# Performance work log

Hardware: AMD Instinct MI355X
Metric: run time of the kernel (lower is better)

Reference implementation:

```python
import jax, jax.numpy as jnp
import numpy as np

NUM_HEADS = 8


def conv2x2_s2(x, w, b):
    # x: [B,C,H,W], w: [O,I,2,2], stride 2, no padding (torch Conv2d k=2,s=2)
    y = jax.lax.conv_general_dilated(
        x, w, window_strides=(2, 2), padding='VALID',
        dimension_numbers=('NCHW', 'OIHW', 'NCHW'))
    return y + b[None, :, None, None]


def up2(x):
    return jnp.repeat(jnp.repeat(x, 2, axis=2), 2, axis=3)


def setup_inputs() -> dict:
    key = jax.random.key(0)
    B, C, H, W = 1, 128, 64, 64
    N = H * W
    ks = jax.random.split(key, 7)
    p = lambda k, shape: jax.random.normal(k, shape, jnp.float32) * 0.02
    return {
        'x': jax.random.normal(ks[0], (B, N, C), jnp.float32),
        'conv1_w': p(ks[1], (C, C, 2, 2)),
        'conv1_b': jnp.zeros((C,), jnp.float32),
        'conv2_w': p(ks[2], (C, C, 2, 2)),
        'conv2_b': jnp.zeros((C,), jnp.float32),
        'q_w': p(ks[3], (C, C)),
        'kv_w': p(ks[4], (2 * C, C)),
        'proj_w': p(ks[5], (C, C)),
        'proj_b': jnp.zeros((C,), jnp.float32),
        'H': H,
        'W': W,
    }


def reference(x, conv1_w, conv1_b, conv2_w, conv2_b, q_w, kv_w, proj_w, proj_b, H, W):
    B, N, C = x.shape
    hd = C // NUM_HEADS
    scale = hd ** -0.5
    # tokens -> feature map
    x_ = x.transpose(0, 2, 1).reshape(B, C, H, W)
    # ChannelPriorQueries: conv(s2) -> up2 -> conv(s2) -> up2 (HxW preserved)
    tq = up2(conv2x2_s2(up2(conv2x2_s2(x_, conv1_w, conv1_b)), conv2_w, conv2_b))
    tq = tq.reshape(B, C, N).transpose(0, 2, 1)  # [B,N,C]
    # projections (torch Linear: y = x @ W.T)
    q = (tq @ q_w.T).reshape(B, N, NUM_HEADS, hd).transpose(0, 2, 1, 3)   # [B,h,N,d]
    kv = (x @ kv_w.T).reshape(B, N, 2, NUM_HEADS, hd).transpose(2, 0, 3, 1, 4)
    k, v = kv[0], kv[1]  # [B,h,N,d]
    # sr_ratio == 1: F.interpolate(q, size=(N, d)) is the identity
    attn = jax.nn.softmax(jnp.einsum('bhqd,bhkd->bhqk', q, k) * scale, axis=-1)
    out = jnp.einsum('bhqk,bhkd->bhqd', attn, v)
    out = out.transpose(0, 2, 1, 3).reshape(B, N, C)
    return out @ proj_w.T + proj_b
```

## Files before the change

### kernel.cpp

```cpp
#include <hip/hip_runtime.h>
#include <hip/hip_bf16.h>

#define CCH 128
#define NTOK 4096
#define NP 1024
#define NH 8
#define HD 16

typedef __attribute__((ext_vector_type(8)))  short s8v;
typedef __attribute__((ext_vector_type(16))) float f32x16;

#define OFF_Y1T   0
#define OFF_M     131072
#define OFF_QB    147456
#define OFF_AT16  147584
#define OFF_K16   180352
#define OFF_VT16  442496

__device__ inline unsigned short f2bf(float v) {
    __hip_bfloat16 b = __float2bfloat16(v);
    return *reinterpret_cast<unsigned short*>(&b);
}
__device__ inline unsigned int pk2bf(float a, float b) {
    __hip_bfloat162 t = __float22bfloat162_rn(make_float2(a, b));
    return *reinterpret_cast<unsigned int*>(&t);
}
__device__ inline int crow_of(int r, int hi) { return (r & 3) + 8*(r >> 2) + 4*hi; }

union BU { unsigned int u[4]; s8v v; };

__global__ void __launch_bounds__(256) kA_prep(const float* __restrict__ x,
        const float* __restrict__ w1, const float* __restrict__ b1,
        const float* __restrict__ w2, const float* __restrict__ b2,
        const float* __restrict__ qw, const float* __restrict__ kvw,
        float* __restrict__ ws,
        unsigned short* __restrict__ k16, unsigned short* __restrict__ vt16) {
    __shared__ float smem[2048];
    const int b = blockIdx.x;
    const int tid = threadIdx.x;
    const int w = tid >> 6, lane = tid & 63;
    const int ql = lane & 31, hi = lane >> 5;

    if (b < 256) {
        const int n0 = (b >> 1) * 32;
        const int octile = (b & 1) * 4 + w;
        const int oc0 = octile * 32;
        const bool isK = (octile < 4);
        const float* arow = (isK ? x + (n0 + ql)*CCH : kvw + (oc0 + ql)*CCH) + hi*8;
        const float* brow = (isK ? kvw + (oc0 + ql)*CCH : x + (n0 + ql)*CCH) + hi*8;
        f32x16 acc = {};
        float4 a0 = *reinterpret_cast<const float4*>(arow);
        float4 a1 = *reinterpret_cast<const float4*>(arow + 4);
        float4 b0 = *reinterpret_cast<const float4*>(brow);
        float4 b1 = *reinterpret_cast<const float4*>(brow + 4);
        for (int kk = 0; kk < 8; ++kk) {
            float4 na0 = a0, na1 = a1, nb0 = b0, nb1 = b1;
            if (kk < 7) {
                na0 = *reinterpret_cast<const float4*>(arow + (kk+1)*16);
                na1 = *reinterpret_cast<const float4*>(arow + (kk+1)*16 + 4);
                nb0 = *reinterpret_cast<const float4*>(brow + (kk+1)*16);
                nb1 = *reinterpret_cast<const float4*>(brow + (kk+1)*16 + 4);
            }
            BU au, bu;
            au.u[0] = pk2bf(a0.x, a0.y); au.u[1] = pk2bf(a0.z, a0.w);
            au.u[2] = pk2bf(a1.x, a1.y); au.u[3] = pk2bf(a1.z, a1.w);
            bu.u[0] = pk2bf(b0.x, b0.y); bu.u[1] = pk2bf(b0.z, b0.w);
            bu.u[2] = pk2bf(b1.x, b1.y); bu.u[3] = pk2bf(b1.z, b1.w);
            acc = __builtin_amdgcn_mfma_f32_32x32x16_bf16(au.v, bu.v, acc, 0, 0, 0);
            a0 = na0; a1 = na1; b0 = nb0; b1 = nb1;
        }
        if (isK) {
            const int oc = oc0 + ql, h = oc >> 4, d = oc & 15;
            #pragma unroll
            for (int r = 0; r < 16; ++r) {
                const int n = n0 + crow_of(r, hi);
                k16[(h*NTOK + n)*HD + d] = f2bf(acc[r]);
            }
        } else {
            #pragma unroll
            for (int r = 0; r < 16; ++r) {
                const int oc = oc0 + crow_of(r, hi);
                vt16[(oc - CCH)*NTOK + n0 + ql] = f2bf(acc[r]);
            }
        }
    } else if (b < 512) {
        const int pp = tid >> 7, o = tid & 127;
        float* xs = smem + pp * 1024;
        const int p0 = (b - 256) * 4 + pp * 2;
        #pragma unroll
        for (int pl = 0; pl < 2; ++pl) {
            int p = p0 + pl;
            int i = p >> 5, j = p & 31;
            int t00 = (2*i)*64 + 2*j;
            float4 v;
            v.x = x[(t00     )*CCH + o];
            v.y = x[(t00 +  1)*CCH + o];
            v.z = x[(t00 + 64)*CCH + o];
            v.w = x[(t00 + 65)*CCH + o];
            *reinterpret_cast<float4*>(&xs[(pl*CCH + o)*4]) = v;
        }
        __syncthreads();
        float acc0 = 0.f, acc1 = 0.f;
        for (int c = 0; c < CCH; ++c) {
            float4 w4 = *reinterpret_cast<const float4*>(&w1[(o*CCH + c)*4]);
            float4 a  = *reinterpret_cast<const float4*>(&xs[c*4]);
            float4 bq = *reinterpret_cast<const float4*>(&xs[(CCH + c)*4]);
            acc0 += w4.x*a.x + w4.y*a.y + w4.z*a.z + w4.w*a.w;
            acc1 += w4.x*bq.x + w4.y*bq.y + w4.z*bq.z + w4.w*bq.w;
        }
        ws[OFF_Y1T + (p0+0)*CCH + o] = acc0 + b1[o];
        ws[OFF_Y1T + (p0+1)*CCH + o] = acc1 + b1[o];
    } else {
        int id = (b - 512) * 256 + tid;
        int r = id >> 7, c = id & 127;
        float acc = 0.f;
        for (int o = 0; o < CCH; ++o) {
            float4 w4 = *reinterpret_cast<const float4*>(&w2[(o*CCH + c)*4]);
            acc += qw[r*CCH + o] * (w4.x + w4.y + w4.z + w4.w);
        }
        ws[OFF_M + id] = acc * 0.25f;
        if (id < CCH) {
            float a = 0.f;
            for (int o = 0; o < CCH; ++o) a += qw[id*CCH + o] * b2[o];
            ws[OFF_QB + id] = a * 0.25f;
        }
    }
}

__global__ void __launch_bounds__(1024) kB_attn(const float* __restrict__ ws,
                                                const unsigned short* __restrict__ k16,
                                                const unsigned short* __restrict__ vt16,
                                                unsigned short* __restrict__ at16) {
    __shared__ float ys[32*CCH];
    __shared__ unsigned short qs[32*24];
    __shared__ float oacc[16*HD*32];
    __shared__ float lbuf[16*32];
    const int tid = threadIdx.x;
    const int h = blockIdx.x >> 5, qt = blockIdx.x & 31;

    reinterpret_cast<float4*>(ys)[tid] =
        reinterpret_cast<const float4*>(ws + OFF_Y1T + qt*32*CCH)[tid];
    __syncthreads();

    {
        const int qq = tid >> 5, r = (tid >> 1) & 15, half = tid & 1;
        const float* Mr = ws + OFF_M + (h*HD + r)*CCH + half*64;
        const float* yr = ys + qq*CCH + half*64;
        float a = 0.f;
        #pragma unroll
        for (int c4 = 0; c4 < 16; ++c4) {
            float4 m4 = *reinterpret_cast<const float4*>(Mr + c4*4);
            float4 y4 = *reinterpret_cast<const float4*>(yr + c4*4);
            a += m4.x*y4.x + m4.y*y4.y + m4.z*y4.z + m4.w*y4.w;
        }
        a += __shfl_xor(a, 1);
        if (half == 0) qs[qq*24 + r] = f2bf(a + ws[OFF_QB + h*HD + r]);
    }
    __syncthreads();

    const int s = tid >> 6;
    const int lane = tid & 63;
    const int ql = lane & 31;
    const int hi = lane >> 5;

    s8v qf = *reinterpret_cast<const s8v*>(qs + ql*24 + hi*8);

    const unsigned short* kp = k16 + (h*NTOK)*HD;
    const unsigned short* vp = vt16 + (h*HD + ql)*NTOK;
    const bool vvalid = (ql < HD);

    f32x16 acc = {};
    float lsum = 0.f;

    const int kbase = s*256;
    s8v kf = *reinterpret_cast<const s8v*>(kp + (kbase + ql)*HD + hi*8);
    s8v vf1 = {}, vf2 = {};
    if (vvalid) {
        vf1 = *reinterpret_cast<const s8v*>(vp + kbase + hi*8);
        vf2 = *reinterpret_cast<const s8v*>(vp + kbase + 16 + hi*8);
    }

    for (int c = 0; c < 8; ++c) {
        s8v kf_n = kf, vf1_n = vf1, vf2_n = vf2;
        if (c < 7) {
            const int kb2 = kbase + (c+1)*32;
            kf_n = *reinterpret_cast<const s8v*>(kp + (kb2 + ql)*HD + hi*8);
            if (vvalid) {
                vf1_n = *reinterpret_cast<const s8v*>(vp + kb2 + hi*8);
                vf2_n = *reinterpret_cast<const s8v*>(vp + kb2 + 16 + hi*8);
            }
        }

        f32x16 z = {};
        f32x16 st = __builtin_amdgcn_mfma_f32_32x32x16_bf16(kf, qf, z, 0, 0, 0);

        float p[16];
        float ls = 0.f;
        #pragma unroll
        for (int r = 0; r < 16; ++r) { p[r] = __expf(st[r]); ls += p[r]; }
        lsum += ls;

        unsigned int W[8];
        #pragma unroll
        for (int i = 0; i < 8; ++i) W[i] = pk2bf(p[2*i], p[2*i+1]);

        BU b1x, b2x;
        {
            unsigned int s0 = (unsigned int)__shfl_xor((int)W[0], 32);
            unsigned int s1 = (unsigned int)__shfl_xor((int)W[1], 32);
            unsigned int s2 = (unsigned int)__shfl_xor((int)W[2], 32);
            unsigned int s3 = (unsigned int)__shfl_xor((int)W[3], 32);
            b1x.u[0] = hi ? s2 : W[0];
            b1x.u[1] = hi ? s3 : W[1];
            b1x.u[2] = hi ? W[2] : s0;
            b1x.u[3] = hi ? W[3] : s1;
            unsigned int s4 = (unsigned int)__shfl_xor((int)W[4], 32);
            unsigned int s5 = (unsigned int)__shfl_xor((int)W[5], 32);
            unsigned int s6 = (unsigned int)__shfl_xor((int)W[6], 32);
            unsigned int s7 = (unsigned int)__shfl_xor((int)W[7], 32);
            b2x.u[0] = hi ? s6 : W[4];
            b2x.u[1] = hi ? s7 : W[5];
            b2x.u[2] = hi ? W[6] : s4;
            b2x.u[3] = hi ? W[7] : s5;
        }

        acc = __builtin_amdgcn_mfma_f32_32x32x16_bf16(vf1, b1x.v, acc, 0, 0, 0);
        acc = __builtin_amdgcn_mfma_f32_32x32x16_bf16(vf2, b2x.v, acc, 0, 0, 0);

        kf = kf_n; vf1 = vf1_n; vf2 = vf2_n;
    }

    float lt = lsum + __shfl_xor(lsum, 32);
    if (lane < 32) lbuf[s*32 + ql] = lt;
    #pragma unroll
    for (int r = 0; r < 8; ++r) {
        int d = crow_of(r, hi);
        oacc[(s*HD + d)*32 + ql] = acc[r];
    }
    __syncthreads();

    if (tid < 512) {
        const int q2 = tid & 31, d2 = tid >> 5;
        float ltot = 0.f, o = 0.f;
        #pragma unroll
        for (int ss = 0; ss < 16; ++ss) {
            ltot += lbuf[ss*32 + q2];
            o    += oacc[(ss*HD + d2)*32 + q2];
        }
        at16[(qt*32 + q2)*CCH + h*HD + d2] = f2bf(o / ltot);
    }
}

__global__ void __launch_bounds__(256) k5_proj(const unsigned short* __restrict__ at16,
                                               const float* __restrict__ pw,
                                               const float* __restrict__ pb,
                                               float* __restrict__ out) {
    const int ptile = blockIdx.x;
    const int w = threadIdx.x >> 6, lane = threadIdx.x & 63;
    const int ql = lane & 31, hi = lane >> 5;
    const int oc0 = w * 32;
    const unsigned short* arow = at16 + (ptile*32 + ql)*CCH + hi*8;
    const float* brow = pw + (oc0 + ql)*CCH + hi*8;

    f32x16 acc = {};
    s8v af = *reinterpret_cast<const s8v*>(arow);
    float4 b0 = *reinterpret_cast<const float4*>(brow);
    float4 b1 = *reinterpret_cast<const float4*>(brow + 4);
    for (int kk = 0; kk < 8; ++kk) {
        s8v naf = af; float4 nb0 = b0, nb1 = b1;
        if (kk < 7) {
            naf = *reinterpret_cast<const s8v*>(arow + (kk+1)*16);
            nb0 = *reinterpret_cast<const float4*>(brow + (kk+1)*16);
            nb1 = *reinterpret_cast<const float4*>(brow + (kk+1)*16 + 4);
        }
        BU bu;
        bu.u[0] = pk2bf(b0.x, b0.y); bu.u[1] = pk2bf(b0.z, b0.w);
        bu.u[2] = pk2bf(b1.x, b1.y); bu.u[3] = pk2bf(b1.z, b1.w);
        acc = __builtin_amdgcn_mfma_f32_32x32x16_bf16(af, bu.v, acc, 0, 0, 0);
        af = naf; b0 = nb0; b1 = nb1;
    }

    const float bias = pb[oc0 + ql];
    #pragma unroll
    for (int r = 0; r < 16; ++r) {
        const int j = crow_of(r, hi);
        const int t00 = 128*ptile + 2*j;
        const float v = acc[r] + bias;
        out[(t00     )*CCH + oc0 + ql] = v;
        out[(t00 +  1)*CCH + oc0 + ql] = v;
        out[(t00 + 64)*CCH + oc0 + ql] = v;
        out[(t00 + 65)*CCH + oc0 + ql] = v;
    }
}

extern "C" void kernel_launch(void* const* d_in, const int* in_sizes, int n_in,
                              void* d_out, int out_size, void* d_ws, size_t ws_size,
                              hipStream_t stream) {
    const float* x   = (const float*)d_in[0];
    const float* w1  = (const float*)d_in[1];
    const float* b1  = (const float*)d_in[2];
    const float* w2  = (const float*)d_in[3];
    const float* b2  = (const float*)d_in[4];
    const float* qw  = (const float*)d_in[5];
    const float* kvw = (const float*)d_in[6];
    const float* pw  = (const float*)d_in[7];
    const float* pb  = (const float*)d_in[8];
    float* ws  = (float*)d_ws;
    float* out = (float*)d_out;

    unsigned short* at16 = (unsigned short*)(ws + OFF_AT16);
    unsigned short* k16  = (unsigned short*)(ws + OFF_K16);
    unsigned short* vt16 = (unsigned short*)(ws + OFF_VT16);

    hipLaunchKernelGGL(kA_prep, dim3(576), dim3(256), 0, stream,
                       x, w1, b1, w2, b2, qw, kvw, ws, k16, vt16);
    hipLaunchKernelGGL(kB_attn, dim3(256), dim3(1024), 0, stream,
                       ws, k16, vt16, at16);
    hipLaunchKernelGGL(k5_proj, dim3(32), dim3(256), 0, stream, at16, pw, pb, out);
}
```

Baseline: 53.10 us.

## Split attention keys across two blocks and merge partial sums in projection

The attention kernel now launches 512 blocks of 512 threads instead of 256 blocks of 1024. Each block handles half of the key range and writes unnormalized partial outputs and row sums in fp32 to workspace. The projection kernel adds the two halves, normalizes, converts to bf16 and runs the GEMM. The aim is more blocks to fill the CUs and a smaller per-block reduction, at the cost of extra fp32 partial traffic, duplicated query-projection work per block, and a projection kernel that no longer prefetches its inputs.

```diff
diff --git a/kernel.cpp b/kernel.cpp
--- a/kernel.cpp
+++ b/kernel.cpp
@@ -13,9 +13,10 @@
 #define OFF_Y1T   0
 #define OFF_M     131072
 #define OFF_QB    147456
-#define OFF_AT16  147584
-#define OFF_K16   180352
-#define OFF_VT16  442496
+#define OFF_ATP   147584
+#define OFF_LP    409728
+#define OFF_K16   426112
+#define OFF_VT16  688256
 
 __device__ inline unsigned short f2bf(float v) {
     __hip_bfloat16 b = __float2bfloat16(v);
@@ -52,9 +53,9 @@
         float4 a0 = *reinterpret_cast<const float4*>(arow);
         float4 a1 = *reinterpret_cast<const float4*>(arow + 4);
         float4 b0 = *reinterpret_cast<const float4*>(brow);
-        float4 b1 = *reinterpret_cast<const float4*>(brow + 4);
+        float4 b1v = *reinterpret_cast<const float4*>(brow + 4);
         for (int kk = 0; kk < 8; ++kk) {
-            float4 na0 = a0, na1 = a1, nb0 = b0, nb1 = b1;
+            float4 na0 = a0, na1 = a1, nb0 = b0, nb1 = b1v;
             if (kk < 7) {
                 na0 = *reinterpret_cast<const float4*>(arow + (kk+1)*16);
                 na1 = *reinterpret_cast<const float4*>(arow + (kk+1)*16 + 4);
@@ -65,9 +66,9 @@
             au.u[0] = pk2bf(a0.x, a0.y); au.u[1] = pk2bf(a0.z, a0.w);
             au.u[2] = pk2bf(a1.x, a1.y); au.u[3] = pk2bf(a1.z, a1.w);
             bu.u[0] = pk2bf(b0.x, b0.y); bu.u[1] = pk2bf(b0.z, b0.w);
-            bu.u[2] = pk2bf(b1.x, b1.y); bu.u[3] = pk2bf(b1.z, b1.w);
+            bu.u[2] = pk2bf(b1v.x, b1v.y); bu.u[3] = pk2bf(b1v.z, b1v.w);
             acc = __builtin_amdgcn_mfma_f32_32x32x16_bf16(au.v, bu.v, acc, 0, 0, 0);
-            a0 = na0; a1 = na1; b0 = nb0; b1 = nb1;
+            a0 = na0; a1 = na1; b0 = nb0; b1v = nb1;
         }
         if (isK) {
             const int oc = oc0 + ql, h = oc >> 4, d = oc & 15;
@@ -127,34 +128,37 @@
     }
 }
 
-__global__ void __launch_bounds__(1024) kB_attn(const float* __restrict__ ws,
-                                                const unsigned short* __restrict__ k16,
-                                                const unsigned short* __restrict__ vt16,
-                                                unsigned short* __restrict__ at16) {
-    __shared__ float ys[32*CCH];
-    __shared__ unsigned short qs[32*24];
-    __shared__ float oacc[16*HD*32];
-    __shared__ float lbuf[16*32];
+__global__ void __launch_bounds__(512) kB_attn(const float* __restrict__ ws,
+                                               const unsigned short* __restrict__ k16,
+                                               const unsigned short* __restrict__ vt16,
+                                               float* __restrict__ atp,
+                                               float* __restrict__ lp) {
+    __shared__ float smem[8832];
+    float* ys = smem;
+    unsigned short* qs = (unsigned short*)(smem + 4096);
+    float* oacc = smem + 4480;
+    float* lbuf = smem + 8576;
     const int tid = threadIdx.x;
-    const int h = blockIdx.x >> 5, qt = blockIdx.x & 31;
-
-    reinterpret_cast<float4*>(ys)[tid] =
-        reinterpret_cast<const float4*>(ws + OFF_Y1T + qt*32*CCH)[tid];
+    const int h = blockIdx.x >> 6, qt = (blockIdx.x >> 1) & 31, kh = blockIdx.x & 1;
+
+    #pragma unroll
+    for (int e = 0; e < 8; ++e)
+        reinterpret_cast<float4*>(ys)[tid + 512*e] =
+            reinterpret_cast<const float4*>(ws + OFF_Y1T + qt*32*CCH)[tid + 512*e];
     __syncthreads();
 
     {
-        const int qq = tid >> 5, r = (tid >> 1) & 15, half = tid & 1;
-        const float* Mr = ws + OFF_M + (h*HD + r)*CCH + half*64;
-        const float* yr = ys + qq*CCH + half*64;
+        const int qq = tid >> 4, r = tid & 15;
+        const float* Mr = ws + OFF_M + (h*HD + r)*CCH;
+        const float* yr = ys + qq*CCH;
         float a = 0.f;
         #pragma unroll
-        for (int c4 = 0; c4 < 16; ++c4) {
+        for (int c4 = 0; c4 < 32; ++c4) {
             float4 m4 = *reinterpret_cast<const float4*>(Mr + c4*4);
             float4 y4 = *reinterpret_cast<const float4*>(yr + c4*4);
             a += m4.x*y4.x + m4.y*y4.y + m4.z*y4.z + m4.w*y4.w;
         }
-        a += __shfl_xor(a, 1);
-        if (half == 0) qs[qq*24 + r] = f2bf(a + ws[OFF_QB + h*HD + r]);
+        qs[qq*24 + r] = f2bf(a + ws[OFF_QB + h*HD + r]);
     }
     __syncthreads();
 
@@ -172,7 +176,7 @@
     f32x16 acc = {};
     float lsum = 0.f;
 
-    const int kbase = s*256;
+    const int kbase = kh*2048 + s*256;
     s8v kf = *reinterpret_cast<const s8v*>(kp + (kbase + ql)*HD + hi*8);
     s8v vf1 = {}, vf2 = {};
     if (vvalid) {
@@ -239,19 +243,22 @@
     }
     __syncthreads();
 
-    if (tid < 512) {
+    {
         const int q2 = tid & 31, d2 = tid >> 5;
         float ltot = 0.f, o = 0.f;
         #pragma unroll
-        for (int ss = 0; ss < 16; ++ss) {
+        for (int ss = 0; ss < 8; ++ss) {
             ltot += lbuf[ss*32 + q2];
             o    += oacc[(ss*HD + d2)*32 + q2];
         }
-        at16[(qt*32 + q2)*CCH + h*HD + d2] = f2bf(o / ltot);
-    }
-}
-
-__global__ void __launch_bounds__(256) k5_proj(const unsigned short* __restrict__ at16,
+        const int p = qt*32 + q2;
+        atp[kh*(NP*CCH) + p*CCH + h*HD + d2] = o;
+        if (d2 == 0) lp[kh*(NP*NH) + p*NH + h] = ltot;
+    }
+}
+
+__global__ void __launch_bounds__(256) k5_proj(const float* __restrict__ atp,
+                                               const float* __restrict__ lp,
                                                const float* __restrict__ pw,
                                                const float* __restrict__ pb,
                                                float* __restrict__ out) {
@@ -259,25 +266,30 @@
     const int w = threadIdx.x >> 6, lane = threadIdx.x & 63;
     const int ql = lane & 31, hi = lane >> 5;
     const int oc0 = w * 32;
-    const unsigned short* arow = at16 + (ptile*32 + ql)*CCH + hi*8;
+    const int p = ptile*32 + ql;
     const float* brow = pw + (oc0 + ql)*CCH + hi*8;
 
     f32x16 acc = {};
-    s8v af = *reinterpret_cast<const s8v*>(arow);
-    float4 b0 = *reinterpret_cast<const float4*>(brow);
-    float4 b1 = *reinterpret_cast<const float4*>(brow + 4);
     for (int kk = 0; kk < 8; ++kk) {
-        s8v naf = af; float4 nb0 = b0, nb1 = b1;
-        if (kk < 7) {
-            naf = *reinterpret_cast<const s8v*>(arow + (kk+1)*16);
-            nb0 = *reinterpret_cast<const float4*>(brow + (kk+1)*16);
-            nb1 = *reinterpret_cast<const float4*>(brow + (kk+1)*16 + 4);
-        }
+        const float l = lp[p*NH + kk] + lp[NP*NH + p*NH + kk];
+        const float rl = 1.f / l;
+        const int base = p*CCH + kk*16 + hi*8;
+        float4 a0 = *reinterpret_cast<const float4*>(atp + base);
+        float4 a1 = *reinterpret_cast<const float4*>(atp + base + 4);
+        float4 c0 = *reinterpret_cast<const float4*>(atp + NP*CCH + base);
+        float4 c1 = *reinterpret_cast<const float4*>(atp + NP*CCH + base + 4);
+        BU af;
+        af.u[0] = pk2bf((a0.x+c0.x)*rl, (a0.y+c0.y)*rl);
+        af.u[1] = pk2bf((a0.z+c0.z)*rl, (a0.w+c0.w)*rl);
+        af.u[2] = pk2bf((a1.x+c1.x)*rl, (a1.y+c1.y)*rl);
+        af.u[3] = pk2bf((a1.z+c1.z)*rl, (a1.w+c1.w)*rl);
+
+        float4 b0 = *reinterpret_cast<const float4*>(brow + kk*16);
+        float4 b1v = *reinterpret_cast<const float4*>(brow + kk*16 + 4);
         BU bu;
         bu.u[0] = pk2bf(b0.x, b0.y); bu.u[1] = pk2bf(b0.z, b0.w);
-        bu.u[2] = pk2bf(b1.x, b1.y); bu.u[3] = pk2bf(b1.z, b1.w);
-        acc = __builtin_amdgcn_mfma_f32_32x32x16_bf16(af, bu.v, acc, 0, 0, 0);
-        af = naf; b0 = nb0; b1 = nb1;
+        bu.u[2] = pk2bf(b1v.x, b1v.y); bu.u[3] = pk2bf(b1v.z, b1v.w);
+        acc = __builtin_amdgcn_mfma_f32_32x32x16_bf16(af.v, bu.v, acc, 0, 0, 0);
     }
 
     const float bias = pb[oc0 + ql];
@@ -308,13 +320,15 @@
     float* ws  = (float*)d_ws;
     float* out = (float*)d_out;
 
-    unsigned short* at16 = (unsigned short*)(ws + OFF_AT16);
+    float* atp = ws + OFF_ATP;
+    float* lp  = ws + OFF_LP;
     unsigned short* k16  = (unsigned short*)(ws + OFF_K16);
     unsigned short* vt16 = (unsigned short*)(ws + OFF_VT16);
 
     hipLaunchKernelGGL(kA_prep, dim3(576), dim3(256), 0, stream,
                        x, w1, b1, w2, b2, qw, kvw, ws, k16, vt16);
-    hipLaunchKernelGGL(kB_attn, dim3(256), dim3(1024), 0, stream,
-                       ws, k16, vt16, at16);
-    hipLaunchKernelGGL(k5_proj, dim3(32), dim3(256), 0, stream, at16, pw, pb, out);
-}
+    hipLaunchKernelGGL(kB_attn, dim3(512), dim3(512), 0, stream,
+                       ws, k16, vt16, atp, lp);
+    hipLaunchKernelGGL(k5_proj, dim3(32), dim3(256), 0, stream,
+                       atp, lp, pw, pb, out);
+}
```

New measurement: 65.79 us. 23.9% more time.
